# Optimization experiments

Hardware: AMD Instinct MI355X
Metric: run time of the kernel (lower is better)

## Reference

```python
import math
import jax, jax.numpy as jnp
import numpy as np

N, M = 2048, 128            # fine grid points, coarse points
IN_NF, H, LMAX = 256, 128, 2
A2B = 1.88973
MIN_STD = 0.32 * A2B / 2.0  # two stddevs reach min covalent radius (Bohr)
MAX_STD = 2.32 * A2B / 2.0


def _sph_lmax2(d):
    # norm-normalized real spherical harmonics (e3nn convention), unit input d[..., 3]
    x, y, z = d[..., 0], d[..., 1], d[..., 2]
    s3 = math.sqrt(3.0)
    sh0 = jnp.ones_like(x)[..., None]                                    # [., 1]
    sh1 = jnp.stack([x, y, z], axis=-1)                                  # [., 3]
    sh2 = jnp.stack([s3 * x * z, s3 * x * y,
                     y * y - 0.5 * (x * x + z * z),
                     s3 * y * z, 0.5 * s3 * (z * z - x * x)], axis=-1)   # [., 5]
    return [sh0, sh1, sh2]


def _radial(dist, nb):
    # Gaussian radial basis; two stddevs span [MIN_COV_RAD, MAX_COV_RAD]
    s = jnp.linspace(MIN_STD, MAX_STD, nb, dtype=dist.dtype)
    temps = 2.0 * s * s
    x2 = dist[..., None] ** 2
    return jnp.exp(-x2 / temps) * (2.0 / 3.0) * x2 / temps / (math.pi * temps) ** 1.5


def setup_inputs():
    key = jax.random.key(0)
    k = jax.random.split(key, 10)
    xav = math.sqrt(6.0 / (H + H))
    return {
        'h': jax.random.normal(k[0], (N, IN_NF), jnp.float32),
        'grid_coords': jax.random.normal(k[1], (N, 3), jnp.float32),
        'coarse_coords': jax.random.normal(k[2], (M, 3), jnp.float32),
        'grid_weights': jax.random.uniform(k[3], (N,), jnp.float32),
        'W_pre': jax.random.normal(k[4], (IN_NF, H), jnp.float32) * math.sqrt(2.0 / (IN_NF + H)),
        'b_pre': jnp.zeros((H,), jnp.float32),
        'W_down': jax.random.uniform(k[5], (LMAX + 1, H, H), jnp.float32, -xav, xav),
        'W_up': jax.random.uniform(k[6], (LMAX + 1, H, H), jnp.float32, -xav, xav),
        'W_post': jax.random.normal(k[7], (H, H), jnp.float32) * math.sqrt(2.0 / (H + H)),
        'b_post': jnp.zeros((H,), jnp.float32),
    }


def reference(h, grid_coords, coarse_coords, grid_weights,
              W_pre, b_pre, W_down, W_up, W_post, b_post):
    h = jax.nn.silu(h @ W_pre + b_pre)                            # [N, H]
    # all-pairs directions/distances (vect_cdist); radius_cutoff = inf -> every pair is an edge
    dvec = grid_coords[:, None, :] - coarse_coords[None, :, :]    # [N, M, 3]
    dist = jnp.sqrt((dvec * dvec + 1e-20).sum(-1))                # [N, M]
    dirs = dvec / dist[..., None]
    sh = _sph_lmax2(dirs)                                         # list of [N, M, 2l+1]
    rad = _radial(dist, H)                                        # [N, M, H]
    # tp_down: paths (0e x le -> le); l=0 uses the scalar branch (no 1/sqrt(2l+1))
    # radial gating per hidden channel + quadrature integration onto coarse nodes
    coarse = []
    for l in range(LMAX + 1):
        norm = 1.0 if l == 0 else math.sqrt(2 * l + 1)
        c = jnp.einsum('nu,uw,nmj,nmw,n->mwj',
                       h, W_down[l], sh[l], rad, grid_weights) / norm
        coarse.append(c)                                          # [M, H, 2l+1]
    # tp_up: paths (le x le -> 0e); l>0 branch divides by sqrt(2l+1); scatter back to grid
    out = 0.0
    for l in range(LMAX + 1):
        norm = 1.0 if l == 0 else math.sqrt(2 * l + 1)
        out = out + jnp.einsum('mui,uw,nmi->nw', coarse[l], W_up[l], sh[l]) / norm
    return jax.nn.silu(out @ W_post + b_post)                     # [N, H]
```

## Files before the change

kernel.cpp:

```cpp
#include <hip/hip_runtime.h>
#include <math.h>

#define N_PTS 2048
#define M_PTS 128
#define INNF  256
#define H     128

#define MIN_STDC 0.30235680f
#define MAX_STDC 2.19208680f
#define PI_F     3.14159265358979f
#define LOG2E_F  1.44269504089f

static __device__ __forceinline__ float silu_f(float x) {
  return x / (1.0f + __expf(-x));
}

__global__ __launch_bounds__(256) void k_pre(const float* __restrict__ h,
    const float* __restrict__ W_pre, const float* __restrict__ b_pre,
    const float* __restrict__ W_down, const float* __restrict__ gw,
    float* __restrict__ hdg4) {
  __shared__ float bigW[12288];
  __shared__ float h_t[8 * INNF];
  __shared__ float hp_t[8 * H];
  int t = threadIdx.x;
  int n0 = blockIdx.x * 8;
  int lw = t & 31;
  int g  = t >> 5;
  int w0 = lw * 4;

  #pragma unroll
  for (int i = 0; i < 2; ++i) {
    int idx = t + i * 256;
    int row = idx >> 6, col = (idx & 63) << 2;
    *(float4*)&h_t[row * INNF + col] =
        *(const float4*)(h + (size_t)(n0 + row) * INNF + col);
  }

  float acc[4] = {};
  for (int kc = 0; kc < 256; kc += 64) {
    __syncthreads();
    #pragma unroll
    for (int i = 0; i < 8; ++i) {
      int idx = t + i * 256;
      *(float4*)&bigW[idx * 4] = *(const float4*)(W_pre + (size_t)kc * H + idx * 4);
    }
    __syncthreads();
    #pragma unroll 4
    for (int u4 = 0; u4 < 16; ++u4) {
      float4 hv = *(const float4*)&h_t[g * INNF + kc + u4 * 4];
      float hvv[4] = {hv.x, hv.y, hv.z, hv.w};
      #pragma unroll
      for (int uu = 0; uu < 4; ++uu) {
        float4 wv = *(const float4*)&bigW[(u4 * 4 + uu) * H + w0];
        acc[0] += hvv[uu] * wv.x; acc[1] += hvv[uu] * wv.y;
        acc[2] += hvv[uu] * wv.z; acc[3] += hvv[uu] * wv.w;
      }
    }
  }
  {
    float4 bv = *(const float4*)(b_pre + w0);
    float4 o = make_float4(silu_f(acc[0] + bv.x), silu_f(acc[1] + bv.y),
                           silu_f(acc[2] + bv.z), silu_f(acc[3] + bv.w));
    __syncthreads();
    *(float4*)&hp_t[g * H + w0] = o;
  }

  float acc2[3][4] = {};
  for (int kc = 0; kc < 128; kc += 32) {
    __syncthreads();
    #pragma unroll
    for (int i = 0; i < 12; ++i) {
      int idx = t + i * 256;
      int l = idx >> 10, r4 = idx & 1023;
      *(float4*)&bigW[idx * 4] =
          *(const float4*)(W_down + ((size_t)l * H + kc) * H + r4 * 4);
    }
    __syncthreads();
    #pragma unroll 2
    for (int u4 = 0; u4 < 8; ++u4) {
      float4 pv = *(const float4*)&hp_t[g * H + kc + u4 * 4];
      float pvv[4] = {pv.x, pv.y, pv.z, pv.w};
      #pragma unroll
      for (int uu = 0; uu < 4; ++uu) {
        int ul = u4 * 4 + uu;
        #pragma unroll
        for (int l = 0; l < 3; ++l) {
          float4 wv = *(const float4*)&bigW[(l * 32 + ul) * H + w0];
          acc2[l][0] += pvv[uu] * wv.x; acc2[l][1] += pvv[uu] * wv.y;
          acc2[l][2] += pvv[uu] * wv.z; acc2[l][3] += pvv[uu] * wv.w;
        }
      }
    }
  }

  {
    const float stp = (MAX_STDC - MIN_STDC) / 127.0f;
    const float invn1 = 0.57735026919f, invn2 = 0.44721359550f;
    int n = n0 + g;
    float gwv = gw[n];
    #pragma unroll
    for (int i = 0; i < 4; ++i) {
      int w = w0 + i;
      float s = MIN_STDC + (float)w * stp;
      float temps = 2.0f * s * s;
      float coef = (2.0f / 3.0f) / (temps * powf(PI_F * temps, 1.5f));
      float sc = gwv * coef;
      *(float4*)(hdg4 + ((size_t)n * H + w) * 4) =
          make_float4(acc2[0][i] * sc, acc2[1][i] * sc * invn1,
                      acc2[2][i] * sc * invn2, 0.0f);
    }
  }
}

__global__ __launch_bounds__(256) void k_down(const float* __restrict__ gc,
    const float* __restrict__ cc, const float* __restrict__ hdg4,
    float* __restrict__ c_part) {
  __shared__ float lds[4608];
  int t = threadIdx.x;
  int m0 = blockIdx.x * 4;
  int ss = blockIdx.y;
  int n0 = ss * 64;
  int w  = t & 127;
  int nh = t >> 7;

  {
    int n_loc = t >> 2, m_loc = t & 3;
    int n = n0 + n_loc, m = m0 + m_loc;
    float dx = gc[3*n]   - cc[3*m];
    float dy = gc[3*n+1] - cc[3*m+1];
    float dz = gc[3*n+2] - cc[3*m+2];
    float d2 = dx*dx + dy*dy + dz*dz + 3e-20f;
    float inv = rsqrtf(d2);
    float x = dx*inv, y = dy*inv, z = dz*inv;
    const float s3 = 1.73205080757f;
    float* dst = &lds[(size_t)t * 12];
    dst[0] = 1.0f; dst[1] = x; dst[2] = y; dst[3] = z;
    dst[4] = s3*x*z; dst[5] = s3*x*y; dst[6] = y*y - 0.5f*(x*x + z*z);
    dst[7] = s3*y*z; dst[8] = 0.5f*s3*(z*z - x*x);
    dst[9] = d2; dst[10] = 0.0f; dst[11] = 0.0f;
  }
  __syncthreads();

  const float stp = (MAX_STDC - MIN_STDC) / 127.0f;
  float sw = MIN_STDC + (float)w * stp;
  float m_nl2t = -LOG2E_F / (2.0f * sw * sw);

  float acc[4][9] = {};
  for (int j = 0; j < 32; j += 4) {
    float4 hv[4];
    #pragma unroll
    for (int q = 0; q < 4; ++q)
      hv[q] = *(const float4*)(hdg4 + ((size_t)(n0 + nh*32 + j + q)*H + w)*4);
    #pragma unroll
    for (int q = 0; q < 4; ++q) {
      const float* shb = &lds[(size_t)(nh*32 + j + q) * 48];
      #pragma unroll
      for (int mm = 0; mm < 4; ++mm) {
        float4 q0 = *(const float4*)(shb + mm*12);
        float4 q1 = *(const float4*)(shb + mm*12 + 4);
        float4 q2 = *(const float4*)(shb + mm*12 + 8);
        float e  = exp2f(q2.y * m_nl2t);
        float rp = e * q2.y;
        float t0 = hv[q].x*rp, t1 = hv[q].y*rp, t2 = hv[q].z*rp;
        acc[mm][0] += t0;
        acc[mm][1] += t1*q0.y; acc[mm][2] += t1*q0.z; acc[mm][3] += t1*q0.w;
        acc[mm][4] += t2*q1.x; acc[mm][5] += t2*q1.y;
        acc[mm][6] += t2*q1.z; acc[mm][7] += t2*q1.w;
        acc[mm][8] += t2*q2.x;
      }
    }
  }

  __syncthreads();
  if (nh == 1) {
    #pragma unroll
    for (int mm = 0; mm < 4; ++mm)
      #pragma unroll
      for (int li = 0; li < 9; ++li)
        lds[(mm*9 + li)*128 + w] = acc[mm][li];
  }
  __syncthreads();
  if (nh == 0) {
    #pragma unroll
    for (int mm = 0; mm < 4; ++mm)
      #pragma unroll
      for (int li = 0; li < 9; ++li) {
        float v = acc[mm][li] + lds[(mm*9 + li)*128 + w];
        c_part[(((size_t)ss*M_PTS + m0 + mm)*9 + li)*H + w] = v;
      }
  }
}

__global__ __launch_bounds__(128) void k_cu(const float* __restrict__ c_part,
    const float* __restrict__ W_up, float* __restrict__ CU9) {
  __shared__ float c_lds[H];
  int t = threadIdx.x;
  int m = blockIdx.x, li = blockIdx.y;
  float v = 0.0f;
  #pragma unroll 8
  for (int s = 0; s < 32; ++s)
    v += c_part[(((size_t)s*M_PTS + m)*9 + li)*H + t];
  c_lds[t] = v;
  __syncthreads();

  int l = (li == 0) ? 0 : (li < 4 ? 1 : 2);
  const float invn[3] = {1.0f, 0.57735026919f, 0.44721359550f};
  float acc = 0.0f;
  for (int u = 0; u < H; u += 4) {
    float w0 = W_up[((size_t)l*H + u + 0)*H + t];
    float w1 = W_up[((size_t)l*H + u + 1)*H + t];
    float w2 = W_up[((size_t)l*H + u + 2)*H + t];
    float w3 = W_up[((size_t)l*H + u + 3)*H + t];
    acc += c_lds[u]*w0 + c_lds[u+1]*w1 + c_lds[u+2]*w2 + c_lds[u+3]*w3;
  }
  CU9[((size_t)m*9 + li)*H + t] = acc * invn[l];
}

__global__ __launch_bounds__(256) void k_up(const float* __restrict__ gc,
    const float* __restrict__ cc, const float* __restrict__ CU9,
    float* __restrict__ out_part) {
  __shared__ float At[72 * 36];
  __shared__ float Bl[72 * 128];
  int t = threadIdx.x;
  int n0 = blockIdx.x * 32;
  int ks = blockIdx.y;
  int wq  = t & 31;
  int tgn = t >> 5;
  int w0 = wq * 4;

  {
    int ch = t >> 7, idx = t & 127;
    int n_loc = idx >> 2, m_loc = idx & 3;
    int mrel = ch*4 + m_loc;
    int n = n0 + n_loc, m = ks*8 + mrel;
    float dx = gc[3*n]   - cc[3*m];
    float dy = gc[3*n+1] - cc[3*m+1];
    float dz = gc[3*n+2] - cc[3*m+2];
    float d2 = dx*dx + dy*dy + dz*dz + 3e-20f;
    float inv = rsqrtf(d2);
    float x = dx*inv, y = dy*inv, z = dz*inv;
    const float s3 = 1.73205080757f;
    float sh[9];
    sh[0] = 1.0f; sh[1] = x; sh[2] = y; sh[3] = z;
    sh[4] = s3*x*z; sh[5] = s3*x*y; sh[6] = y*y - 0.5f*(x*x + z*z);
    sh[7] = s3*y*z; sh[8] = 0.5f*s3*(z*z - x*x);
    #pragma unroll
    for (int li = 0; li < 9; ++li)
      At[(mrel*9 + li)*36 + n_loc] = sh[li];
  }
  #pragma unroll
  for (int i = 0; i < 9; ++i) {
    int idx = t + i*256;
    *(float4*)&Bl[idx*4] = *(const float4*)(CU9 + (size_t)ks*72*H + idx*4);
  }
  __syncthreads();

  float acc[4][4] = {};
  #pragma unroll 8
  for (int k = 0; k < 72; ++k) {
    float4 a = *(const float4*)&At[k*36 + 4*tgn];
    float4 b = *(const float4*)&Bl[k*128 + w0];
    float av[4] = {a.x, a.y, a.z, a.w};
    float bv[4] = {b.x, b.y, b.z, b.w};
    #pragma unroll
    for (int r = 0; r < 4; ++r)
      #pragma unroll
      for (int c = 0; c < 4; ++c)
        acc[r][c] += av[r] * bv[c];
  }
  #pragma unroll
  for (int r = 0; r < 4; ++r) {
    size_t row = (size_t)ks*N_PTS + n0 + 4*tgn + r;
    *(float4*)(out_part + row*H + w0) =
        make_float4(acc[r][0], acc[r][1], acc[r][2], acc[r][3]);
  }
}

__global__ __launch_bounds__(256) void k_post(const float* __restrict__ out_part,
    const float* __restrict__ W_post, const float* __restrict__ b_post,
    float* __restrict__ out) {
  __shared__ float op[4 * H];
  int t = threadIdx.x;
  int n0 = blockIdx.x * 4;
  int w = t & 127, nh = t >> 7;

  #pragma unroll
  for (int i = 0; i < 2; ++i) {
    int idx = t + i*256;
    int nl = idx >> 7, ww = idx & 127;
    float v = 0.0f;
    #pragma unroll
    for (int s = 0; s < 16; ++s)
      v += out_part[((size_t)s*N_PTS + n0 + nl)*H + ww];
    op[nl*H + ww] = v;
  }
  __syncthreads();

  float acc[2] = {0.0f, 0.0f};
  for (int u = 0; u < H; u += 4) {
    float4 p0 = *(const float4*)&op[(nh*2 + 0)*H + u];
    float4 p1 = *(const float4*)&op[(nh*2 + 1)*H + u];
    float w0 = W_post[(u+0)*H + w];
    float w1 = W_post[(u+1)*H + w];
    float w2 = W_post[(u+2)*H + w];
    float w3 = W_post[(u+3)*H + w];
    acc[0] += p0.x*w0 + p0.y*w1 + p0.z*w2 + p0.w*w3;
    acc[1] += p1.x*w0 + p1.y*w1 + p1.z*w2 + p1.w*w3;
  }
  float bp = b_post[w];
  out[(size_t)(n0 + nh*2 + 0)*H + w] = silu_f(acc[0] + bp);
  out[(size_t)(n0 + nh*2 + 1)*H + w] = silu_f(acc[1] + bp);
}

extern "C" void kernel_launch(void* const* d_in, const int* in_sizes, int n_in,
                              void* d_out, int out_size, void* d_ws, size_t ws_size,
                              hipStream_t stream) {
  const float* h      = (const float*)d_in[0];
  const float* gc     = (const float*)d_in[1];
  const float* cc     = (const float*)d_in[2];
  const float* gw     = (const float*)d_in[3];
  const float* W_pre  = (const float*)d_in[4];
  const float* b_pre  = (const float*)d_in[5];
  const float* W_down = (const float*)d_in[6];
  const float* W_up   = (const float*)d_in[7];
  const float* W_post = (const float*)d_in[8];
  const float* b_post = (const float*)d_in[9];

  float* ws       = (float*)d_ws;
  float* hdg4     = ws;
  float* c_part   = hdg4 + 1048576;
  float* CU9      = c_part + 4718592;
  float* out_part = c_part;
  float* out      = (float*)d_out;

  k_pre <<<256,           256, 0, stream>>>(h, W_pre, b_pre, W_down, gw, hdg4);
  k_down<<<dim3(32,32),   256, 0, stream>>>(gc, cc, hdg4, c_part);
  k_cu  <<<dim3(128,9),   128, 0, stream>>>(c_part, W_up, CU9);
  k_up  <<<dim3(64,16),   256, 0, stream>>>(gc, cc, CU9, out_part);
  k_post<<<512,           256, 0, stream>>>(out_part, W_post, b_post, out);
}
```

Before: 147.3 us.

## Retile k_down to two channels per thread and enlarge k_up output tiles

k_down now gives each thread two hidden channels and splits the 64 grid points across four wavefronts instead of two halves. This lets each thread reuse the spherical-harmonic LDS reads across two channels. The partial sums are then combined with a two-stage LDS tree reduction. k_up doubles its block tile to 64 points with 4x8 register tiles per thread and halves the grid, improving operand reuse per LDS load. The trade-off is higher register pressure (72 accumulators in k_down, 32 in k_up), more LDS use, extra barriers, and fewer blocks for k_up.

```diff
diff --git a/kernel.cpp b/kernel.cpp
--- a/kernel.cpp
+++ b/kernel.cpp
@@ -115,13 +115,15 @@
 __global__ __launch_bounds__(256) void k_down(const float* __restrict__ gc,
     const float* __restrict__ cc, const float* __restrict__ hdg4,
     float* __restrict__ c_part) {
-  __shared__ float lds[4608];
+  __shared__ float sh_t[3072];
+  __shared__ float red[9216];
   int t = threadIdx.x;
   int m0 = blockIdx.x * 4;
   int ss = blockIdx.y;
   int n0 = ss * 64;
-  int w  = t & 127;
-  int nh = t >> 7;
+  int wv = t >> 6;
+  int ln = t & 63;
+  int w0 = ln * 2;
 
   {
     int n_loc = t >> 2, m_loc = t & 3;
@@ -133,7 +135,7 @@
     float inv = rsqrtf(d2);
     float x = dx*inv, y = dy*inv, z = dz*inv;
     const float s3 = 1.73205080757f;
-    float* dst = &lds[(size_t)t * 12];
+    float* dst = &sh_t[(size_t)t * 12];
     dst[0] = 1.0f; dst[1] = x; dst[2] = y; dst[3] = z;
     dst[4] = s3*x*z; dst[5] = s3*x*y; dst[6] = y*y - 0.5f*(x*x + z*z);
     dst[7] = s3*y*z; dst[8] = 0.5f*s3*(z*z - x*x);
@@ -142,51 +144,79 @@
   __syncthreads();
 
   const float stp = (MAX_STDC - MIN_STDC) / 127.0f;
-  float sw = MIN_STDC + (float)w * stp;
-  float m_nl2t = -LOG2E_F / (2.0f * sw * sw);
-
-  float acc[4][9] = {};
-  for (int j = 0; j < 32; j += 4) {
-    float4 hv[4];
-    #pragma unroll
-    for (int q = 0; q < 4; ++q)
-      hv[q] = *(const float4*)(hdg4 + ((size_t)(n0 + nh*32 + j + q)*H + w)*4);
-    #pragma unroll
-    for (int q = 0; q < 4; ++q) {
-      const float* shb = &lds[(size_t)(nh*32 + j + q) * 48];
-      #pragma unroll
-      for (int mm = 0; mm < 4; ++mm) {
-        float4 q0 = *(const float4*)(shb + mm*12);
-        float4 q1 = *(const float4*)(shb + mm*12 + 4);
-        float4 q2 = *(const float4*)(shb + mm*12 + 8);
-        float e  = exp2f(q2.y * m_nl2t);
-        float rp = e * q2.y;
-        float t0 = hv[q].x*rp, t1 = hv[q].y*rp, t2 = hv[q].z*rp;
-        acc[mm][0] += t0;
-        acc[mm][1] += t1*q0.y; acc[mm][2] += t1*q0.z; acc[mm][3] += t1*q0.w;
-        acc[mm][4] += t2*q1.x; acc[mm][5] += t2*q1.y;
-        acc[mm][6] += t2*q1.z; acc[mm][7] += t2*q1.w;
-        acc[mm][8] += t2*q2.x;
+  float sA = MIN_STDC + (float)w0 * stp;
+  float sB = MIN_STDC + (float)(w0 + 1) * stp;
+  float cA = -LOG2E_F / (2.0f * sA * sA);
+  float cB = -LOG2E_F / (2.0f * sB * sB);
+
+  float acc[4][9][2] = {};
+  for (int j = 0; j < 16; ++j) {
+    int nl = wv * 16 + j;
+    const float4* hb = (const float4*)(hdg4 + ((size_t)(n0 + nl) * H + w0) * 4);
+    float4 hv0 = hb[0];
+    float4 hv1 = hb[1];
+    const float* shb = &sh_t[(size_t)nl * 48];
+    #pragma unroll
+    for (int mm = 0; mm < 4; ++mm) {
+      float4 q0 = *(const float4*)(shb + mm*12);
+      float4 q1 = *(const float4*)(shb + mm*12 + 4);
+      float4 q2 = *(const float4*)(shb + mm*12 + 8);
+      float e0 = exp2f(q2.y * cA);
+      float e1 = exp2f(q2.y * cB);
+      float rp0 = e0 * q2.y, rp1 = e1 * q2.y;
+      float a00 = hv0.x*rp0, a01 = hv0.y*rp0, a02 = hv0.z*rp0;
+      float a10 = hv1.x*rp1, a11 = hv1.y*rp1, a12 = hv1.z*rp1;
+      acc[mm][0][0] += a00;        acc[mm][0][1] += a10;
+      acc[mm][1][0] += a01*q0.y;   acc[mm][1][1] += a11*q0.y;
+      acc[mm][2][0] += a01*q0.z;   acc[mm][2][1] += a11*q0.z;
+      acc[mm][3][0] += a01*q0.w;   acc[mm][3][1] += a11*q0.w;
+      acc[mm][4][0] += a02*q1.x;   acc[mm][4][1] += a12*q1.x;
+      acc[mm][5][0] += a02*q1.y;   acc[mm][5][1] += a12*q1.y;
+      acc[mm][6][0] += a02*q1.z;   acc[mm][6][1] += a12*q1.z;
+      acc[mm][7][0] += a02*q1.w;   acc[mm][7][1] += a12*q1.w;
+      acc[mm][8][0] += a02*q2.x;   acc[mm][8][1] += a12*q2.x;
+    }
+  }
+
+  __syncthreads();
+  if (wv & 1) {
+    float* dst = &red[(wv >> 1) * 4608];
+    #pragma unroll
+    for (int mm = 0; mm < 4; ++mm)
+      #pragma unroll
+      for (int li = 0; li < 9; ++li)
+        *(float2*)&dst[(mm*9 + li)*128 + w0] =
+            make_float2(acc[mm][li][0], acc[mm][li][1]);
+  }
+  __syncthreads();
+  if (!(wv & 1)) {
+    const float* src = &red[(wv >> 1) * 4608];
+    #pragma unroll
+    for (int mm = 0; mm < 4; ++mm)
+      #pragma unroll
+      for (int li = 0; li < 9; ++li) {
+        float2 v = *(const float2*)&src[(mm*9 + li)*128 + w0];
+        acc[mm][li][0] += v.x; acc[mm][li][1] += v.y;
       }
-    }
-  }
-
-  __syncthreads();
-  if (nh == 1) {
+  }
+  __syncthreads();
+  if (wv == 2) {
     #pragma unroll
     for (int mm = 0; mm < 4; ++mm)
       #pragma unroll
       for (int li = 0; li < 9; ++li)
-        lds[(mm*9 + li)*128 + w] = acc[mm][li];
-  }
-  __syncthreads();
-  if (nh == 0) {
+        *(float2*)&red[(mm*9 + li)*128 + w0] =
+            make_float2(acc[mm][li][0], acc[mm][li][1]);
+  }
+  __syncthreads();
+  if (wv == 0) {
     #pragma unroll
     for (int mm = 0; mm < 4; ++mm)
       #pragma unroll
       for (int li = 0; li < 9; ++li) {
-        float v = acc[mm][li] + lds[(mm*9 + li)*128 + w];
-        c_part[(((size_t)ss*M_PTS + m0 + mm)*9 + li)*H + w] = v;
+        float2 v = *(const float2*)&red[(mm*9 + li)*128 + w0];
+        float2 o = make_float2(acc[mm][li][0] + v.x, acc[mm][li][1] + v.y);
+        *(float2*)&c_part[(((size_t)ss*M_PTS + m0 + mm)*9 + li)*H + w0] = o;
       }
   }
 }
@@ -219,19 +249,19 @@
 __global__ __launch_bounds__(256) void k_up(const float* __restrict__ gc,
     const float* __restrict__ cc, const float* __restrict__ CU9,
     float* __restrict__ out_part) {
-  __shared__ float At[72 * 36];
+  __shared__ float At[72 * 68];
   __shared__ float Bl[72 * 128];
   int t = threadIdx.x;
-  int n0 = blockIdx.x * 32;
+  int n0 = blockIdx.x * 64;
   int ks = blockIdx.y;
-  int wq  = t & 31;
-  int tgn = t >> 5;
-  int w0 = wq * 4;
-
-  {
-    int ch = t >> 7, idx = t & 127;
-    int n_loc = idx >> 2, m_loc = idx & 3;
-    int mrel = ch*4 + m_loc;
+  int wq  = t & 15;
+  int tgn = t >> 4;
+  int w0 = wq * 8;
+
+  #pragma unroll
+  for (int i = 0; i < 2; ++i) {
+    int idx = t + i * 256;
+    int n_loc = idx >> 3, mrel = idx & 7;
     int n = n0 + n_loc, m = ks*8 + mrel;
     float dx = gc[3*n]   - cc[3*m];
     float dy = gc[3*n+1] - cc[3*m+1];
@@ -246,7 +276,7 @@
     sh[7] = s3*y*z; sh[8] = 0.5f*s3*(z*z - x*x);
     #pragma unroll
     for (int li = 0; li < 9; ++li)
-      At[(mrel*9 + li)*36 + n_loc] = sh[li];
+      At[(mrel*9 + li)*68 + n_loc] = sh[li];
   }
   #pragma unroll
   for (int i = 0; i < 9; ++i) {
@@ -255,17 +285,18 @@
   }
   __syncthreads();
 
-  float acc[4][4] = {};
+  float acc[4][8] = {};
   #pragma unroll 8
   for (int k = 0; k < 72; ++k) {
-    float4 a = *(const float4*)&At[k*36 + 4*tgn];
-    float4 b = *(const float4*)&Bl[k*128 + w0];
+    float4 a  = *(const float4*)&At[k*68 + 4*tgn];
+    float4 b0 = *(const float4*)&Bl[k*128 + w0];
+    float4 b1 = *(const float4*)&Bl[k*128 + w0 + 4];
     float av[4] = {a.x, a.y, a.z, a.w};
-    float bv[4] = {b.x, b.y, b.z, b.w};
+    float bv[8] = {b0.x, b0.y, b0.z, b0.w, b1.x, b1.y, b1.z, b1.w};
     #pragma unroll
     for (int r = 0; r < 4; ++r)
       #pragma unroll
-      for (int c = 0; c < 4; ++c)
+      for (int c = 0; c < 8; ++c)
         acc[r][c] += av[r] * bv[c];
   }
   #pragma unroll
@@ -273,6 +304,8 @@
     size_t row = (size_t)ks*N_PTS + n0 + 4*tgn + r;
     *(float4*)(out_part + row*H + w0) =
         make_float4(acc[r][0], acc[r][1], acc[r][2], acc[r][3]);
+    *(float4*)(out_part + row*H + w0 + 4) =
+        make_float4(acc[r][4], acc[r][5], acc[r][6], acc[r][7]);
   }
 }
 
@@ -336,6 +369,6 @@
   k_pre <<<256,           256, 0, stream>>>(h, W_pre, b_pre, W_down, gw, hdg4);
   k_down<<<dim3(32,32),   256, 0, stream>>>(gc, cc, hdg4, c_part);
   k_cu  <<<dim3(128,9),   128, 0, stream>>>(c_part, W_up, CU9);
-  k_up  <<<dim3(64,16),   256, 0, stream>>>(gc, cc, CU9, out_part);
+  k_up  <<<dim3(32,16),   256, 0, stream>>>(gc, cc, CU9, out_part);
   k_post<<<512,           256, 0, stream>>>(out_part, W_post, b_post, out);
 }
```

Measured after the change: 145.8 us. Within noise of the previous version (-1.0%).
